# Kernel optimization log

Hardware: AMD Instinct MI355X
Metric: run time of the kernel (lower is better)

## Reference

```python
import jax, jax.numpy as jnp
import numpy as np

EMBED_DIM = 1024
NUM_HEADS = 16
HEAD_DIM = EMBED_DIM // NUM_HEADS


def setup_inputs() -> dict:
    key = jax.random.key(0)
    ks = jax.random.split(key, 10)
    s = 1.0 / np.sqrt(EMBED_DIM)
    inp = {
        "x1": jax.random.normal(ks[0], (4, 1024, EMBED_DIM), jnp.float32),
        "x2": jax.random.normal(ks[1], (4, 2048, EMBED_DIM), jnp.float32),
        "Wq": jax.random.normal(ks[2], (EMBED_DIM, EMBED_DIM), jnp.float32) * s,
        "bq": jnp.zeros((EMBED_DIM,), jnp.float32),
        "Wk": jax.random.normal(ks[3], (EMBED_DIM, EMBED_DIM), jnp.float32) * s,
        "bk": jnp.zeros((EMBED_DIM,), jnp.float32),
        "Wv": jax.random.normal(ks[4], (EMBED_DIM, EMBED_DIM), jnp.float32) * s,
        "bv": jnp.zeros((EMBED_DIM,), jnp.float32),
        "Wo": jax.random.normal(ks[5], (EMBED_DIM, EMBED_DIM), jnp.float32) * s,
        "bo": jnp.zeros((EMBED_DIM,), jnp.float32),
    }
    return inp


def reference(x1, x2, Wq, bq, Wk, bk, Wv, bv, Wo, bo):
    B, Sq, E = x1.shape
    Skv = x2.shape[1]
    H, D = NUM_HEADS, HEAD_DIM
    # linear projections (PyTorch Linear: x @ W.T + b)
    q = (x1 @ Wq.T + bq).reshape(B, Sq, H, D).transpose(0, 2, 1, 3)   # [B,H,Sq,D]
    k = (x2 @ Wk.T + bk).reshape(B, Skv, H, D).transpose(0, 2, 1, 3)  # [B,H,Skv,D]
    v = (x2 @ Wv.T + bv).reshape(B, Skv, H, D).transpose(0, 2, 1, 3)
    scores = jnp.einsum("bhqd,bhkd->bhqk", q, k) / jnp.sqrt(jnp.float32(D))
    attn = jax.nn.softmax(scores, axis=-1)
    out = jnp.einsum("bhqk,bhkd->bhqd", attn, v)
    out = out.transpose(0, 2, 1, 3).reshape(B, Sq, E)
    return out @ Wo.T + bo
```

## Files before the change

kernel.cpp:

```cpp
#include <hip/hip_runtime.h>

typedef __attribute__((ext_vector_type(8))) short short8;
typedef __attribute__((ext_vector_type(4))) short short4v;
typedef __attribute__((ext_vector_type(4))) float f32x4;

#define ASYNC16(g, l) __builtin_amdgcn_global_load_lds( \
    (__attribute__((address_space(1))) void*)(g), \
    (__attribute__((address_space(3))) void*)(l), 16, 0, 0)

__device__ __forceinline__ short f2bf(float f) {
  union { float f; unsigned u; } v; v.f = f;
  unsigned r = v.u + 0x7fffu + ((v.u >> 16) & 1u);
  return (short)(r >> 16);
}

__device__ __forceinline__ unsigned pack_bf2(float lo, float hi) {
  union { float f; unsigned u; } a, b; a.f = lo; b.f = hi;
  return __builtin_amdgcn_perm(b.u + 0x8000u, a.u + 0x8000u, 0x07060302u);
}

__device__ __forceinline__ f32x4 fzero4() {
  f32x4 z; z[0] = 0.f; z[1] = 0.f; z[2] = 0.f; z[3] = 0.f; return z;
}

__device__ __forceinline__ void wg_barrier() {
  asm volatile("s_waitcnt lgkmcnt(0)\n\ts_barrier" ::: "memory");
}

__global__ __launch_bounds__(256) void cvt_all(
    const float* __restrict__ x1, const float* __restrict__ x2,
    const float* __restrict__ wq, const float* __restrict__ wk,
    const float* __restrict__ wv, const float* __restrict__ wo,
    short* __restrict__ dst) {
  long e = ((long)blockIdx.x * 256 + threadIdx.x) * 4;
  const float* src; long loc;
  if (e < 4194304L)       { src = x1; loc = e; }
  else if (e < 12582912L) { src = x2; loc = e - 4194304L; }
  else if (e < 13631488L) { src = wq; loc = e - 12582912L; }
  else if (e < 14680064L) { src = wk; loc = e - 13631488L; }
  else if (e < 15728640L) { src = wv; loc = e - 14680064L; }
  else                    { src = wo; loc = e - 15728640L; }
  float4 v = *(const float4*)(src + loc);
  short4v o;
  o[0] = f2bf(v.x); o[1] = f2bf(v.y); o[2] = f2bf(v.z); o[3] = f2bf(v.w);
  *(short4v*)(dst + e) = o;
}

__global__ __launch_bounds__(256) void proj(
    const short* __restrict__ xb1, const short* __restrict__ xb2,
    const short* __restrict__ wqp, const short* __restrict__ wkp, const short* __restrict__ wvp,
    const float* __restrict__ bq, const float* __restrict__ bk, const float* __restrict__ bv,
    short* __restrict__ qb, short* __restrict__ kb, short* __restrict__ vb) {
  __shared__ short smem[16384];
  short* As = smem;
  short* Bs = smem + 4096;
  const int tid = threadIdx.x, w = tid >> 6, lane = tid & 63;
  const int quad = lane >> 4, col = lane & 15;
  const int waveM = (w >> 1) * 64, waveN = (w & 1) * 64;
  const int my = blockIdx.x, bn = blockIdx.y * 128;
  const short* A; const short* W; const float* bias; int mode, bm;
  if (my < 32)      { A = xb1; W = wqp; bias = bq; mode = 0; bm = my * 128; }
  else if (my < 96) { A = xb2; W = wkp; bias = bk; mode = 1; bm = (my - 32) * 128; }
  else              { A = xb2; W = wvp; bias = bv; mode = 2; bm = (my - 96) * 128; }

  f32x4 acc[4][4];
  for (int mi = 0; mi < 4; ++mi)
    for (int ni = 0; ni < 4; ++ni)
      acc[mi][ni] = fzero4();

  const int srow = w * 16 + (lane >> 2), scol = (lane & 3) * 8;
  const short* ga = A + (size_t)(bm + srow) * 1024 + scol;
  const short* gb = W + (size_t)(bn + srow) * 1024 + scol;
  short* lA = As + w * 512;
  short* lB = Bs + w * 512;

  for (int kk = 0; kk < 1024; kk += 32) {
    __syncthreads();
    ASYNC16(ga + kk,         lA);
    ASYNC16(ga + kk + 65536, lA + 2048);
    ASYNC16(gb + kk,         lB);
    ASYNC16(gb + kk + 65536, lB + 2048);
    __syncthreads();
    short8 af[4], bf[4];
    for (int mi = 0; mi < 4; ++mi)
      af[mi] = *(const short8*)(As + (waveM + mi * 16 + col) * 32 + quad * 8);
    for (int ni = 0; ni < 4; ++ni)
      bf[ni] = *(const short8*)(Bs + (waveN + ni * 16 + col) * 32 + quad * 8);
    for (int mi = 0; mi < 4; ++mi)
      for (int ni = 0; ni < 4; ++ni)
        acc[mi][ni] = __builtin_amdgcn_mfma_f32_16x16x32_bf16(af[mi], bf[ni], acc[mi][ni], 0, 0, 0);
  }

  __syncthreads();
  for (int ni = 0; ni < 4; ++ni) {
    int nn = waveN + ni * 16 + col;
    float bvl = bias[bn + nn];
    for (int mi = 0; mi < 4; ++mi) {
      int m0 = waveM + mi * 16 + quad * 4;
      for (int r = 0; r < 4; ++r) {
        int m = m0 + r;
        smem[m * 128 + (nn ^ ((m & 15) << 3))] = f2bf(acc[mi][ni][r] + bvl);
      }
    }
  }
  __syncthreads();
  if (mode < 2) {
    const int S = (mode == 0) ? 1024 : 2048;
    short* outp = (mode == 0) ? qb : kb;
    const int bb = bm / S, s0 = bm & (S - 1), h0 = bn >> 6;
    for (int it = 0; it < 8; ++it) {
      int f = (it * 256 + tid) * 8;
      int hh = f >> 13, rem = f & 8191, m = rem >> 6, d = rem & 63;
      int nn = hh * 64 + d;
      short8 val = *(const short8*)&smem[m * 128 + (nn ^ ((m & 15) << 3))];
      *(short8*)(outp + ((((size_t)(bb * 16 + h0 + hh)) * S + s0 + m) * 64 + d)) = val;
    }
  } else {
    const int bb = bm >> 11, s0 = bm & 2047, kt0 = s0 >> 6, h0 = bn >> 6;
    for (int it = 0; it < 8; ++it) {
      int f = (it * 256 + tid) * 8;
      int hh = f >> 13, rem = f & 8191, ktl = rem >> 12, r3 = rem & 4095;
      int d = r3 >> 6, kvp0 = r3 & 63;
      int nn = hh * 64 + d;
      short8 val;
      for (int j = 0; j < 8; ++j) {
        int kvp = kvp0 + j;
        int kv = ((kvp & 3) << 4) | (kvp >> 2);
        int m = ktl * 64 + kv;
        val[j] = smem[m * 128 + (nn ^ ((m & 15) << 3))];
      }
      *(short8*)(vb + ((((size_t)(bb * 16 + h0 + hh)) * 32 + (kt0 + ktl)) * 4096) + d * 64 + kvp0) = val;
    }
  }
}

__global__ __launch_bounds__(256) void out_gemm(
    const short* __restrict__ A, const short* __restrict__ W,
    const float* __restrict__ bias, float* __restrict__ out) {
  __shared__ short As[4096];
  __shared__ short Bs[4096];
  const int tid = threadIdx.x, w = tid >> 6, lane = tid & 63;
  const int quad = lane >> 4, col = lane & 15;
  const int waveM = (w >> 1) * 64, waveN = (w & 1) * 64;
  const int bm = blockIdx.x * 128, bn = blockIdx.y * 128;

  f32x4 acc[4][4];
  for (int mi = 0; mi < 4; ++mi)
    for (int ni = 0; ni < 4; ++ni)
      acc[mi][ni] = fzero4();

  const int srow = tid >> 1, sc0 = (tid & 1) * 16;
  const short* ga = A + (size_t)(bm + srow) * 1024 + sc0;
  const short* gb = W + (size_t)(bn + srow) * 1024 + sc0;

  short8 a0 = *(const short8*)ga,       a1 = *(const short8*)(ga + 8);
  short8 b0 = *(const short8*)gb,       b1 = *(const short8*)(gb + 8);

  for (int kk = 0; kk < 1024; kk += 32) {
    wg_barrier();
    *(short8*)&As[srow * 32 + sc0]     = a0;
    *(short8*)&As[srow * 32 + sc0 + 8] = a1;
    *(short8*)&Bs[srow * 32 + sc0]     = b0;
    *(short8*)&Bs[srow * 32 + sc0 + 8] = b1;
    int kn = (kk < 992) ? kk + 32 : kk;
    a0 = *(const short8*)(ga + kn); a1 = *(const short8*)(ga + kn + 8);
    b0 = *(const short8*)(gb + kn); b1 = *(const short8*)(gb + kn + 8);
    wg_barrier();
    short8 af[4], bf[4];
    for (int mi = 0; mi < 4; ++mi)
      af[mi] = *(const short8*)(As + (waveM + mi * 16 + col) * 32 + quad * 8);
    for (int ni = 0; ni < 4; ++ni)
      bf[ni] = *(const short8*)(Bs + (waveN + ni * 16 + col) * 32 + quad * 8);
    for (int mi = 0; mi < 4; ++mi)
      for (int ni = 0; ni < 4; ++ni)
        acc[mi][ni] = __builtin_amdgcn_mfma_f32_16x16x32_bf16(af[mi], bf[ni], acc[mi][ni], 0, 0, 0);
  }

  for (int ni = 0; ni < 4; ++ni) {
    int n = bn + waveN + ni * 16 + col;
    float bvl = bias[n];
    for (int mi = 0; mi < 4; ++mi) {
      int m0 = bm + waveM + mi * 16 + quad * 4;
      for (int r = 0; r < 4; ++r)
        out[(size_t)(m0 + r) * 1024 + n] = acc[mi][ni][r] + bvl;
    }
  }
}

__global__ __launch_bounds__(256) void attn(
    const short* __restrict__ Q, const short* __restrict__ K,
    const short* __restrict__ V, short* __restrict__ O) {
  __shared__ short Ks[64 * 72];
  __shared__ short Vs[64 * 72];
  __shared__ short Ps[128 * 72];
  const int tid = threadIdx.x, w = tid >> 6, lane = tid & 63;
  const int quad = lane >> 4, col = lane & 15;
  const int bh = blockIdx.x, qt = blockIdx.y;
  const int b = bh >> 4, h = bh & 15;
  const int qbase = w * 32;

  const short* qp = Q + ((size_t)bh * 1024 + qt * 128) * 64;
  const short* kp = K + (size_t)bh * 131072;
  const short* vp = V + (size_t)bh * 131072;

  short8 aq[2][2];
  for (int mi = 0; mi < 2; ++mi) {
    const short* qr = qp + (qbase + mi * 16 + col) * 64 + quad * 8;
    aq[mi][0] = *(const short8*)qr;
    aq[mi][1] = *(const short8*)(qr + 32);
  }

  float lsum[2][4];
  f32x4 oa[2][4];
  for (int mi = 0; mi < 2; ++mi) {
    for (int r = 0; r < 4; ++r) lsum[mi][r] = 0.f;
    for (int ni = 0; ni < 4; ++ni) oa[mi][ni] = fzero4();
  }

  const int sr = tid >> 2, sc0 = (tid & 3) * 16;
  const float c = 0.18033688011112042f;

  short8 k0 = *(const short8*)(kp + tid * 16), k1 = *(const short8*)(kp + tid * 16 + 8);
  short8 v0 = *(const short8*)(vp + tid * 16), v1 = *(const short8*)(vp + tid * 16 + 8);

  for (int kt = 0; kt < 32; ++kt) {
    wg_barrier();
    *(short8*)&Ks[sr * 72 + sc0]     = k0;
    *(short8*)&Ks[sr * 72 + sc0 + 8] = k1;
    *(short8*)&Vs[sr * 72 + sc0]     = v0;
    *(short8*)&Vs[sr * 72 + sc0 + 8] = v1;
    {
      int ktn = (kt < 31) ? kt + 1 : kt;
      const short* kg = kp + ktn * 4096 + tid * 16;
      const short* vg = vp + ktn * 4096 + tid * 16;
      k0 = *(const short8*)kg; k1 = *(const short8*)(kg + 8);
      v0 = *(const short8*)vg; v1 = *(const short8*)(vg + 8);
    }
    wg_barrier();

    short8 bk0[4], bk1[4];
    for (int nk = 0; nk < 4; ++nk) {
      bk0[nk] = *(const short8*)&Ks[(nk * 16 + col) * 72 + quad * 8];
      bk1[nk] = *(const short8*)&Ks[(nk * 16 + col) * 72 + 32 + quad * 8];
    }
    f32x4 sf[2][4];
    for (int mi = 0; mi < 2; ++mi)
      for (int nk = 0; nk < 4; ++nk) {
        f32x4 z = fzero4();
        z = __builtin_amdgcn_mfma_f32_16x16x32_bf16(aq[mi][0], bk0[nk], z, 0, 0, 0);
        z = __builtin_amdgcn_mfma_f32_16x16x32_bf16(aq[mi][1], bk1[nk], z, 0, 0, 0);
        sf[mi][nk] = z;
      }

    for (int mi = 0; mi < 2; ++mi)
      for (int nk = 0; nk < 4; ++nk)
        for (int r = 0; r < 4; ++r)
          sf[mi][nk][r] = __builtin_amdgcn_exp2f(sf[mi][nk][r] * c);
    for (int mi = 0; mi < 2; ++mi)
      for (int r = 0; r < 4; ++r)
        lsum[mi][r] += (sf[mi][0][r] + sf[mi][1][r]) + (sf[mi][2][r] + sf[mi][3][r]);

    for (int mi = 0; mi < 2; ++mi)
      for (int r = 0; r < 4; ++r) {
        uint2 d;
        d.x = pack_bf2(sf[mi][0][r], sf[mi][1][r]);
        d.y = pack_bf2(sf[mi][2][r], sf[mi][3][r]);
        *(uint2*)&Ps[(qbase + mi * 16 + quad * 4 + r) * 72 + col * 4] = d;
      }

    short8 bv0[4], bv1[4];
    for (int ni = 0; ni < 4; ++ni) {
      bv0[ni] = *(const short8*)&Vs[(ni * 16 + col) * 72 + quad * 8];
      bv1[ni] = *(const short8*)&Vs[(ni * 16 + col) * 72 + 32 + quad * 8];
    }
    for (int mi = 0; mi < 2; ++mi) {
      short8 ap0 = *(const short8*)&Ps[(qbase + mi * 16 + col) * 72 + quad * 8];
      short8 ap1 = *(const short8*)&Ps[(qbase + mi * 16 + col) * 72 + 32 + quad * 8];
      for (int ni = 0; ni < 4; ++ni) {
        oa[mi][ni] = __builtin_amdgcn_mfma_f32_16x16x32_bf16(ap0, bv0[ni], oa[mi][ni], 0, 0, 0);
        oa[mi][ni] = __builtin_amdgcn_mfma_f32_16x16x32_bf16(ap1, bv1[ni], oa[mi][ni], 0, 0, 0);
      }
    }
  }

  for (int mi = 0; mi < 2; ++mi)
    for (int r = 0; r < 4; ++r) {
      float s = lsum[mi][r];
      s += __shfl_xor(s, 1);
      s += __shfl_xor(s, 2);
      s += __shfl_xor(s, 4);
      s += __shfl_xor(s, 8);
      lsum[mi][r] = 1.f / s;
    }
  __syncthreads();
  for (int mi = 0; mi < 2; ++mi)
    for (int ni = 0; ni < 4; ++ni)
      for (int r = 0; r < 4; ++r)
        Ps[(qbase + mi * 16 + quad * 4 + r) * 64 + ni * 16 + col] = f2bf(oa[mi][ni][r] * lsum[mi][r]);
  __syncthreads();
  for (int it = 0; it < 4; ++it) {
    int f = (it * 256 + tid) * 8;
    int q = f >> 6, d = f & 63;
    short8 val = *(const short8*)&Ps[q * 64 + d];
    *(short8*)(O + ((size_t)(b * 1024 + qt * 128 + q)) * 1024 + h * 64 + d) = val;
  }
}

extern "C" void kernel_launch(void* const* d_in, const int* in_sizes, int n_in,
                              void* d_out, int out_size, void* d_ws, size_t ws_size,
                              hipStream_t stream) {
  const float* x1 = (const float*)d_in[0];
  const float* x2 = (const float*)d_in[1];
  const float* Wq = (const float*)d_in[2];
  const float* bq = (const float*)d_in[3];
  const float* Wk = (const float*)d_in[4];
  const float* bk = (const float*)d_in[5];
  const float* Wv = (const float*)d_in[6];
  const float* bv = (const float*)d_in[7];
  const float* Wo = (const float*)d_in[8];
  const float* bo = (const float*)d_in[9];

  char* ws = (char*)d_ws;
  short* xb1 = (short*)(ws + 0);
  short* xb2 = (short*)(ws + 8388608);
  short* wqb = (short*)(ws + 25165824);
  short* wkb = (short*)(ws + 27262976);
  short* wvb = (short*)(ws + 29360128);
  short* wob = (short*)(ws + 31457280);
  short* qb  = (short*)(ws + 33554432);
  short* kb  = (short*)(ws + 41943040);
  short* vb  = (short*)(ws + 58720256);
  short* ob  = (short*)(ws + 75497472);

  cvt_all<<<16384, 256, 0, stream>>>(x1, x2, Wq, Wk, Wv, Wo, (short*)ws);
  proj<<<dim3(160, 8), 256, 0, stream>>>(xb1, xb2, wqb, wkb, wvb, bq, bk, bv, qb, kb, vb);
  attn<<<dim3(64, 8), 256, 0, stream>>>(qb, kb, vb, ob);
  out_gemm<<<dim3(32, 8), 256, 0, stream>>>(ob, wob, bo, (float*)d_out);
}
```

Baseline: 241.7 us.

## Double attention KV tile to 128 and shrink out_gemm tiles with async LDS loads

The attention kernel now handles 128 keys per iteration instead of 64. This halves the loop trips and barriers, and it streams V slices with a wider padded layout. It is also given a two-blocks-per-CU launch bound, at the cost of more LDS and register pressure. The output GEMM moves to 64x128 tiles on a larger grid to fill more CUs, and it loads tiles with global_load_lds async copies instead of register staging. The GEMM loses the software prefetch overlap, because each load is now waited on by barriers within the same iteration.

```diff
diff --git a/kernel.cpp b/kernel.cpp
--- a/kernel.cpp
+++ b/kernel.cpp
@@ -137,41 +137,35 @@
 __global__ __launch_bounds__(256) void out_gemm(
     const short* __restrict__ A, const short* __restrict__ W,
     const float* __restrict__ bias, float* __restrict__ out) {
-  __shared__ short As[4096];
-  __shared__ short Bs[4096];
+  __shared__ short As[64 * 32];
+  __shared__ short Bs[128 * 32];
   const int tid = threadIdx.x, w = tid >> 6, lane = tid & 63;
   const int quad = lane >> 4, col = lane & 15;
-  const int waveM = (w >> 1) * 64, waveN = (w & 1) * 64;
-  const int bm = blockIdx.x * 128, bn = blockIdx.y * 128;
-
-  f32x4 acc[4][4];
-  for (int mi = 0; mi < 4; ++mi)
+  const int waveM = (w >> 1) * 32, waveN = (w & 1) * 64;
+  const int bn = blockIdx.x * 128, bm = blockIdx.y * 64;
+
+  f32x4 acc[2][4];
+  for (int mi = 0; mi < 2; ++mi)
     for (int ni = 0; ni < 4; ++ni)
       acc[mi][ni] = fzero4();
 
-  const int srow = tid >> 1, sc0 = (tid & 1) * 16;
-  const short* ga = A + (size_t)(bm + srow) * 1024 + sc0;
-  const short* gb = W + (size_t)(bn + srow) * 1024 + sc0;
-
-  short8 a0 = *(const short8*)ga,       a1 = *(const short8*)(ga + 8);
-  short8 b0 = *(const short8*)gb,       b1 = *(const short8*)(gb + 8);
+  const short* ga = A + (size_t)(bm + (tid >> 2)) * 1024 + (tid & 3) * 8;
+  const short* gb = W + (size_t)(bn + (tid >> 2)) * 1024 + (tid & 3) * 8;
+  short* lA = As + w * 512;
+  short* lB = Bs + w * 512;
 
   for (int kk = 0; kk < 1024; kk += 32) {
-    wg_barrier();
-    *(short8*)&As[srow * 32 + sc0]     = a0;
-    *(short8*)&As[srow * 32 + sc0 + 8] = a1;
-    *(short8*)&Bs[srow * 32 + sc0]     = b0;
-    *(short8*)&Bs[srow * 32 + sc0 + 8] = b1;
-    int kn = (kk < 992) ? kk + 32 : kk;
-    a0 = *(const short8*)(ga + kn); a1 = *(const short8*)(ga + kn + 8);
-    b0 = *(const short8*)(gb + kn); b1 = *(const short8*)(gb + kn + 8);
-    wg_barrier();
-    short8 af[4], bf[4];
-    for (int mi = 0; mi < 4; ++mi)
+    __syncthreads();
+    ASYNC16(ga + kk,         lA);
+    ASYNC16(gb + kk,         lB);
+    ASYNC16(gb + kk + 65536, lB + 2048);
+    __syncthreads();
+    short8 af[2], bf[4];
+    for (int mi = 0; mi < 2; ++mi)
       af[mi] = *(const short8*)(As + (waveM + mi * 16 + col) * 32 + quad * 8);
     for (int ni = 0; ni < 4; ++ni)
       bf[ni] = *(const short8*)(Bs + (waveN + ni * 16 + col) * 32 + quad * 8);
-    for (int mi = 0; mi < 4; ++mi)
+    for (int mi = 0; mi < 2; ++mi)
       for (int ni = 0; ni < 4; ++ni)
         acc[mi][ni] = __builtin_amdgcn_mfma_f32_16x16x32_bf16(af[mi], bf[ni], acc[mi][ni], 0, 0, 0);
   }
@@ -179,7 +173,7 @@
   for (int ni = 0; ni < 4; ++ni) {
     int n = bn + waveN + ni * 16 + col;
     float bvl = bias[n];
-    for (int mi = 0; mi < 4; ++mi) {
+    for (int mi = 0; mi < 2; ++mi) {
       int m0 = bm + waveM + mi * 16 + quad * 4;
       for (int r = 0; r < 4; ++r)
         out[(size_t)(m0 + r) * 1024 + n] = acc[mi][ni][r] + bvl;
@@ -187,12 +181,12 @@
   }
 }
 
-__global__ __launch_bounds__(256) void attn(
+__global__ __launch_bounds__(256, 2) void attn(
     const short* __restrict__ Q, const short* __restrict__ K,
     const short* __restrict__ V, short* __restrict__ O) {
-  __shared__ short Ks[64 * 72];
-  __shared__ short Vs[64 * 72];
-  __shared__ short Ps[128 * 72];
+  __shared__ short Ks[128 * 72];
+  __shared__ short Vs[64 * 136];
+  __shared__ short Ps[128 * 136];
   const int tid = threadIdx.x, w = tid >> 6, lane = tid & 63;
   const int quad = lane >> 4, col = lane & 15;
   const int bh = blockIdx.x, qt = blockIdx.y;
@@ -217,68 +211,69 @@
     for (int ni = 0; ni < 4; ++ni) oa[mi][ni] = fzero4();
   }
 
-  const int sr = tid >> 2, sc0 = (tid & 3) * 16;
+  const int krow = lane + (w >> 1) * 64, kch = (w & 1) * 32;
+  const int vd = lane, vch = w & 1, vkh = (w >> 1) * 32;
   const float c = 0.18033688011112042f;
 
-  short8 k0 = *(const short8*)(kp + tid * 16), k1 = *(const short8*)(kp + tid * 16 + 8);
-  short8 v0 = *(const short8*)(vp + tid * 16), v1 = *(const short8*)(vp + tid * 16 + 8);
-
-  for (int kt = 0; kt < 32; ++kt) {
+  short8 kpre[4], vpre[4];
+  {
+    const short* kg = kp + krow * 64 + kch;
+    const short* vg = vp + vch * 4096 + vd * 64 + vkh;
+    for (int i = 0; i < 4; ++i) kpre[i] = *(const short8*)(kg + i * 8);
+    for (int i = 0; i < 4; ++i) vpre[i] = *(const short8*)(vg + i * 8);
+  }
+
+  for (int kt = 0; kt < 16; ++kt) {
     wg_barrier();
-    *(short8*)&Ks[sr * 72 + sc0]     = k0;
-    *(short8*)&Ks[sr * 72 + sc0 + 8] = k1;
-    *(short8*)&Vs[sr * 72 + sc0]     = v0;
-    *(short8*)&Vs[sr * 72 + sc0 + 8] = v1;
+    for (int i = 0; i < 4; ++i)
+      *(short8*)&Ks[krow * 72 + kch + i * 8] = kpre[i];
+    for (int i = 0; i < 4; ++i)
+      *(short8*)&Vs[vd * 136 + vch * 64 + vkh + i * 8] = vpre[i];
     {
-      int ktn = (kt < 31) ? kt + 1 : kt;
-      const short* kg = kp + ktn * 4096 + tid * 16;
-      const short* vg = vp + ktn * 4096 + tid * 16;
-      k0 = *(const short8*)kg; k1 = *(const short8*)(kg + 8);
-      v0 = *(const short8*)vg; v1 = *(const short8*)(vg + 8);
+      int ktn = (kt < 15) ? kt + 1 : kt;
+      const short* kg = kp + ktn * 8192 + krow * 64 + kch;
+      const short* vg = vp + (2 * ktn + vch) * 4096 + vd * 64 + vkh;
+      for (int i = 0; i < 4; ++i) kpre[i] = *(const short8*)(kg + i * 8);
+      for (int i = 0; i < 4; ++i) vpre[i] = *(const short8*)(vg + i * 8);
     }
     wg_barrier();
 
-    short8 bk0[4], bk1[4];
-    for (int nk = 0; nk < 4; ++nk) {
-      bk0[nk] = *(const short8*)&Ks[(nk * 16 + col) * 72 + quad * 8];
-      bk1[nk] = *(const short8*)&Ks[(nk * 16 + col) * 72 + 32 + quad * 8];
-    }
-    f32x4 sf[2][4];
-    for (int mi = 0; mi < 2; ++mi)
-      for (int nk = 0; nk < 4; ++nk) {
+    for (int mi = 0; mi < 2; ++mi) {
+      f32x4 sf[8];
+      for (int nk = 0; nk < 8; ++nk) {
+        short8 bk0 = *(const short8*)&Ks[(nk * 16 + col) * 72 + quad * 8];
+        short8 bk1 = *(const short8*)&Ks[(nk * 16 + col) * 72 + 32 + quad * 8];
         f32x4 z = fzero4();
-        z = __builtin_amdgcn_mfma_f32_16x16x32_bf16(aq[mi][0], bk0[nk], z, 0, 0, 0);
-        z = __builtin_amdgcn_mfma_f32_16x16x32_bf16(aq[mi][1], bk1[nk], z, 0, 0, 0);
-        sf[mi][nk] = z;
-      }
-
-    for (int mi = 0; mi < 2; ++mi)
-      for (int nk = 0; nk < 4; ++nk)
+        z = __builtin_amdgcn_mfma_f32_16x16x32_bf16(aq[mi][0], bk0, z, 0, 0, 0);
+        z = __builtin_amdgcn_mfma_f32_16x16x32_bf16(aq[mi][1], bk1, z, 0, 0, 0);
+        sf[nk] = z;
+      }
+      for (int nk = 0; nk < 8; ++nk)
         for (int r = 0; r < 4; ++r)
-          sf[mi][nk][r] = __builtin_amdgcn_exp2f(sf[mi][nk][r] * c);
-    for (int mi = 0; mi < 2; ++mi)
+          sf[nk][r] = __builtin_amdgcn_exp2f(sf[nk][r] * c);
       for (int r = 0; r < 4; ++r)
-        lsum[mi][r] += (sf[mi][0][r] + sf[mi][1][r]) + (sf[mi][2][r] + sf[mi][3][r]);
-
-    for (int mi = 0; mi < 2; ++mi)
+        lsum[mi][r] += ((sf[0][r] + sf[1][r]) + (sf[2][r] + sf[3][r])) +
+                       ((sf[4][r] + sf[5][r]) + (sf[6][r] + sf[7][r]));
       for (int r = 0; r < 4; ++r) {
-        uint2 d;
-        d.x = pack_bf2(sf[mi][0][r], sf[mi][1][r]);
-        d.y = pack_bf2(sf[mi][2][r], sf[mi][3][r]);
-        *(uint2*)&Ps[(qbase + mi * 16 + quad * 4 + r) * 72 + col * 4] = d;
-      }
-
-    short8 bv0[4], bv1[4];
-    for (int ni = 0; ni < 4; ++ni) {
-      bv0[ni] = *(const short8*)&Vs[(ni * 16 + col) * 72 + quad * 8];
-      bv1[ni] = *(const short8*)&Vs[(ni * 16 + col) * 72 + 32 + quad * 8];
-    }
-    for (int mi = 0; mi < 2; ++mi) {
-      short8 ap0 = *(const short8*)&Ps[(qbase + mi * 16 + col) * 72 + quad * 8];
-      short8 ap1 = *(const short8*)&Ps[(qbase + mi * 16 + col) * 72 + 32 + quad * 8];
+        int row = qbase + mi * 16 + quad * 4 + r;
+        uint2 d0, d1;
+        d0.x = pack_bf2(sf[0][r], sf[1][r]);
+        d0.y = pack_bf2(sf[2][r], sf[3][r]);
+        d1.x = pack_bf2(sf[4][r], sf[5][r]);
+        d1.y = pack_bf2(sf[6][r], sf[7][r]);
+        *(uint2*)&Ps[row * 136 + col * 4]      = d0;
+        *(uint2*)&Ps[row * 136 + 64 + col * 4] = d1;
+      }
+    }
+
+    for (int ks = 0; ks < 4; ++ks) {
+      int koff = ks * 32 + quad * 8;
+      short8 ap0 = *(const short8*)&Ps[(qbase + col) * 136 + koff];
+      short8 ap1 = *(const short8*)&Ps[(qbase + 16 + col) * 136 + koff];
       for (int ni = 0; ni < 4; ++ni) {
-        oa[mi][ni] = __builtin_amdgcn_mfma_f32_16x16x32_bf16(ap0, bv0[ni], oa[mi][ni], 0, 0, 0);
-        oa[mi][ni] = __builtin_amdgcn_mfma_f32_16x16x32_bf16(ap1, bv1[ni], oa[mi][ni], 0, 0, 0);
+        short8 bv = *(const short8*)&Vs[(ni * 16 + col) * 136 + koff];
+        oa[0][ni] = __builtin_amdgcn_mfma_f32_16x16x32_bf16(ap0, bv, oa[0][ni], 0, 0, 0);
+        oa[1][ni] = __builtin_amdgcn_mfma_f32_16x16x32_bf16(ap1, bv, oa[1][ni], 0, 0, 0);
       }
     }
   }
@@ -335,5 +330,5 @@
   cvt_all<<<16384, 256, 0, stream>>>(x1, x2, Wq, Wk, Wv, Wo, (short*)ws);
   proj<<<dim3(160, 8), 256, 0, stream>>>(xb1, xb2, wqb, wkb, wvb, bq, bk, bv, qb, kb, vb);
   attn<<<dim3(64, 8), 256, 0, stream>>>(qb, kb, vb, ob);
-  out_gemm<<<dim3(32, 8), 256, 0, stream>>>(ob, wob, bo, (float*)d_out);
-}
+  out_gemm<<<dim3(8, 64), 256, 0, stream>>>(ob, wob, bo, (float*)d_out);
+}
```

Result: no change. 246.2 us (+1.9%).
